# Kernel tuning notes

Measured on AMD Instinct MI355X. Metric: run time of the kernel, lower is better.

Reference implementation:

```python
import jax, jax.numpy as jnp
import numpy as np

LN_EPS = 1e-4
NEG = -1e10


def setup_inputs() -> dict:
    key = jax.random.key(0)
    ks = jax.random.split(key, 5)
    b, p, d, i, h, m = 2, 2048, 1024, 16, 64, 4096
    sd = 1.0 / np.sqrt(d)
    return {
        "x": jax.random.normal(ks[0], (b, p, d), jnp.float32),
        "W_K": jax.random.normal(ks[1], (i, h, d), jnp.float32) * sd,
        "W_Q": jax.random.normal(ks[2], (i, h, d), jnp.float32) * sd,
        "W_V": jax.random.normal(ks[3], (i, h, d), jnp.float32) * sd,
        "w_ln": jnp.ones((d,), jnp.float32),
        "b_ln": jnp.zeros((d,), jnp.float32),
        "W_in": jax.random.normal(ks[4], (m, d), jnp.float32) * sd,
        "b_in": jnp.zeros((m,), jnp.float32),
        "W_out": jax.random.normal(jax.random.fold_in(key, 9), (d, m), jnp.float32) * sd,
        "b_out": jnp.zeros((d,), jnp.float32),
    }


def reference(x, W_K, W_Q, W_V, w_ln, b_ln, W_in, b_in, W_out, b_out):
    b, p, d = x.shape
    # --- attention (unscaled softmax, scaled=False in TransformerBlock) ---
    k = jnp.einsum('ihd,bpd->biph', W_K, x)
    q = jnp.einsum('ihd,bpd->biph', W_Q, x)
    v = jnp.einsum('ihd,bpd->biph', W_V, x)
    scores = jnp.einsum('biph,biqh->biqp', k, q)  # [b,i,q_pos,k_pos]
    causal = jnp.tril(jnp.ones((p, p), bool))      # k_pos <= q_pos
    masked = jnp.where(causal, scores, NEG)
    attn = jax.nn.softmax(masked, axis=-1)
    z = jnp.einsum('biph,biqp->biqh', v, attn)     # [b,i,q,h]
    z_flat = jnp.transpose(z, (0, 2, 1, 3)).reshape(b, p, d)  # b q (i h)
    x = x + z_flat
    # --- custom LayerNorm: unbiased std, eps added to std ---
    c = x - jnp.mean(x, axis=-1, keepdims=True)
    std = jnp.sqrt(jnp.sum(c * c, axis=-1, keepdims=True) / (d - 1))
    x = c / (std + LN_EPS) * w_ln + b_ln
    # --- MLP with residual ---
    hpre = jnp.einsum('md,bpd->bpm', W_in, x) + b_in
    hact = jax.nn.gelu(hpre, approximate=False)
    mlp = jnp.einsum('dm,bpm->bpd', W_out, hact) + b_out
    return x + mlp
```

## Files before the change

kernel.cpp:

```cpp
#include <hip/hip_runtime.h>
#include <hip/hip_bf16.h>

typedef __bf16 bf16x8 __attribute__((ext_vector_type(8)));
typedef float f32x4 __attribute__((ext_vector_type(4)));

#define BAR() __builtin_amdgcn_s_barrier()
#define MEMFENCE() asm volatile("" ::: "memory")
#define VMCNT8() asm volatile("s_waitcnt vmcnt(8)" ::: "memory")
#define VMCNT6() asm volatile("s_waitcnt vmcnt(6)" ::: "memory")
#define VMCNT2() asm volatile("s_waitcnt vmcnt(2)" ::: "memory")
#define VMCNT0() asm volatile("s_waitcnt vmcnt(0)" ::: "memory")

__device__ __forceinline__ void gload_lds16(const void* g, void* l) {
  __builtin_amdgcn_global_load_lds(
      (const __attribute__((address_space(1))) void*)g,
      (__attribute__((address_space(3))) void*)l, 16, 0, 0);
}

__global__ __launch_bounds__(256) void k_f2b_all(
    const float* __restrict__ x, const float* __restrict__ wk,
    const float* __restrict__ wq, const float* __restrict__ wv,
    const float* __restrict__ wi, const float* __restrict__ wo,
    __bf16* __restrict__ xb, __bf16* __restrict__ wqkv,
    __bf16* __restrict__ winb, __bf16* __restrict__ woutb) {
  int i = (blockIdx.x * 256 + threadIdx.x) * 4;
  const float* s; __bf16* d; int off;
  if (i < 4194304)       { s = x;  d = xb;             off = i; }
  else if (i < 5242880)  { s = wk; d = wqkv;           off = i - 4194304; }
  else if (i < 6291456)  { s = wq; d = wqkv + 1048576; off = i - 5242880; }
  else if (i < 7340032)  { s = wv; d = wqkv + 2097152; off = i - 6291456; }
  else if (i < 11534336) { s = wi; d = winb;           off = i - 7340032; }
  else                   { s = wo; d = woutb;          off = i - 11534336; }
  const float4 v = *(const float4*)(s + off);
  d[off + 0] = (__bf16)v.x;
  d[off + 1] = (__bf16)v.y;
  d[off + 2] = (__bf16)v.z;
  d[off + 3] = (__bf16)v.w;
}

template <int EPI, int WM, int WN, int MI, int NI, int SMT, int SNT>
__global__ __launch_bounds__(WM * WN * 64, 2) void k_gemm(
    const __bf16* __restrict__ A, const __bf16* __restrict__ B, int N, int K,
    int NT, const float* __restrict__ bias, const float* __restrict__ resid,
    float* __restrict__ outf, __bf16* __restrict__ outb,
    __bf16* __restrict__ ok, __bf16* __restrict__ oq, __bf16* __restrict__ ovt) {
  constexpr int BM = WM * MI * 16, BN = WN * NI * 16;
  constexpr int LA = BM / (8 * WM * WN);
  constexpr int LB = BN / (8 * WM * WN);
  __shared__ __align__(16) __bf16 lds[2][(BM + BN) * 64];
  const int tid = threadIdx.x;
  const int lane = tid & 63, wid = tid >> 6;
  const int wr = wid / WN, wc = wid % WN;
  const int lr = lane & 15, lh = lane >> 4;
  const int bid = blockIdx.x;
  const int cpx = gridDim.x >> 3;
  const int sid = (bid & 7) * cpx + (bid >> 3);
  const int stn = NT / SNT;
  const int stile = sid / (SMT * SNT);
  const int within = sid - stile * (SMT * SNT);
  const int mt = (stile / stn) * SMT + within / SNT;
  const int nt = (stile % stn) * SNT + within % SNT;
  const int m0 = mt * BM, n0 = nt * BN;
  const int nkt = K >> 6;

  auto stage = [&](int t, int bufi) {
    const int k0 = t << 6;
    __bf16* As = lds[bufi];
    __bf16* Bs = lds[bufi] + BM * 64;
#pragma unroll
    for (int j = 0; j < LA; ++j) {
      int chunk = (wid * LA + j) * 64 + lane;
      int row = chunk >> 3, c8 = chunk & 7;
      int g8 = c8 ^ (row & 7);
      gload_lds16(A + (size_t)(m0 + row) * K + k0 + g8 * 8, As + chunk * 8);
    }
#pragma unroll
    for (int j = 0; j < LB; ++j) {
      int chunk = (wid * LB + j) * 64 + lane;
      int row = chunk >> 3, c8 = chunk & 7;
      int g8 = c8 ^ (row & 7);
      gload_lds16(B + (size_t)(n0 + row) * K + k0 + g8 * 8, Bs + chunk * 8);
    }
  };

  f32x4 acc[MI][NI] = {};
  stage(0, 0);
  stage(1, 1);
  if constexpr (LA + LB == 8) { VMCNT8(); } else { VMCNT6(); }
  BAR();

  for (int t = 0; t < nkt; ++t) {
    const __bf16* As = lds[t & 1];
    const __bf16* Bs = lds[t & 1] + BM * 64;
#pragma unroll
    for (int ks = 0; ks < 2; ++ks) {
      bf16x8 af[MI], bf[NI];
#pragma unroll
      for (int mi = 0; mi < MI; ++mi) {
        int row = wr * (MI * 16) + mi * 16 + lr;
        af[mi] = *(const bf16x8*)&As[row * 64 + (((ks * 4 + lh) ^ (row & 7)) * 8)];
      }
#pragma unroll
      for (int ni = 0; ni < NI; ++ni) {
        int row = wc * (NI * 16) + ni * 16 + lr;
        bf[ni] = *(const bf16x8*)&Bs[row * 64 + (((ks * 4 + lh) ^ (row & 7)) * 8)];
      }
#pragma unroll
      for (int mi = 0; mi < MI; ++mi)
#pragma unroll
        for (int ni = 0; ni < NI; ++ni)
          acc[mi][ni] = __builtin_amdgcn_mfma_f32_16x16x32_bf16(
              af[mi], bf[ni], acc[mi][ni], 0, 0, 0);
    }
    MEMFENCE();
    BAR();
    if (t + 2 < nkt) {
      stage(t + 2, t & 1);
      if constexpr (LA + LB == 8) { VMCNT8(); } else { VMCNT6(); }
    } else {
      VMCNT0();
    }
    BAR();
  }

#pragma unroll
  for (int mi = 0; mi < MI; ++mi) {
#pragma unroll
    for (int j = 0; j < 4; ++j) {
      const int row = m0 + wr * (MI * 16) + mi * 16 + lh * 4 + j;
#pragma unroll
      for (int ni = 0; ni < NI; ++ni) {
        const int col = n0 + wc * (NI * 16) + ni * 16 + lr;
        float v = acc[mi][ni][j];
        if constexpr (EPI == 0) {
          const int which = col >> 10, c = col & 1023;
          const int ih = c >> 6, hh = c & 63;
          const int bb = row >> 11, pp = row & 2047;
          const int bi = bb * 16 + ih;
          if (which == 0)
            ok[((size_t)bi * 2048 + pp) * 64 + hh] = (__bf16)v;
          else if (which == 1)
            oq[((size_t)bi * 2048 + pp) * 64 + hh] = (__bf16)v;
          else
            ovt[((size_t)bi * 64 + hh) * 2048 + pp] = (__bf16)v;
        } else if constexpr (EPI == 1) {
          float h = v + bias[col];
          float g = 0.5f * h * (1.f + erff(h * 0.70710678118f));
          outb[(size_t)row * N + col] = (__bf16)g;
        } else {
          outf[(size_t)row * N + col] = v + bias[col] + resid[(size_t)row * N + col];
        }
      }
    }
  }
}

__global__ __launch_bounds__(512) void k_attn(const __bf16* __restrict__ kb,
                                              const __bf16* __restrict__ qb,
                                              const __bf16* __restrict__ vt,
                                              float* __restrict__ z) {
  const int tid = threadIdx.x;
  const int lane = tid & 63, w = tid >> 6;
  const int lr = lane & 15, lh = lane >> 4;
  const int wgid = blockIdx.x;
  const int xcd = wgid & 7;
  const int t = wgid >> 3;
  const int bi = xcd + 8 * (t & 3);
  const int qblk = t >> 2;
  const int b = bi >> 4, ih = bi & 15;
  const int q0B = qblk * 256;
  const int qw = q0B + w * 32;
  const __bf16* kbase = kb + (size_t)bi * 2048 * 64;
  const __bf16* qbase = qb + (size_t)bi * 2048 * 64;
  const __bf16* vbase = vt + (size_t)bi * 64 * 2048;

  __shared__ __align__(16) __bf16 kv[2][2][64 * 64];
  __shared__ __align__(16) __bf16 plds[8][2][16 * 76];

  const int nk = (q0B >> 6) + 4;

  auto stage = [&](int kt, int bufi) {
    const int k0 = kt << 6;
    const int row = tid >> 3, c8 = tid & 7;
    const int g8 = c8 ^ (row & 7);
    gload_lds16(kbase + (size_t)(k0 + row) * 64 + g8 * 8,
                &kv[bufi][0][tid * 8]);
    gload_lds16(vbase + (size_t)row * 2048 + k0 + g8 * 8,
                &kv[bufi][1][tid * 8]);
  };

  bf16x8 aq[2][2];
#pragma unroll
  for (int tl = 0; tl < 2; ++tl)
#pragma unroll
    for (int ks = 0; ks < 2; ++ks)
      aq[tl][ks] = *(const bf16x8*)(qbase + (size_t)(qw + tl * 16 + lr) * 64 + ks * 32 + lh * 8);

  f32x4 o[2][4] = {};
  float lsum[2][4] = {};

  stage(0, 0);
  stage(1, 1);
  VMCNT2();
  BAR();

  for (int kt = 0; kt < nk; ++kt) {
    const int k0 = kt << 6;
    const __bf16* Ks = kv[kt & 1][0];
    const __bf16* Vs = kv[kt & 1][1];
    const bool act = (k0 <= qw + 31);

    if (act) {
      bf16x8 bk[4][2];
#pragma unroll
      for (int n = 0; n < 4; ++n) {
        int r = n * 16 + lr;
#pragma unroll
        for (int ks = 0; ks < 2; ++ks)
          bk[n][ks] = *(const bf16x8*)&Ks[r * 64 + (((ks * 4 + lh) ^ (r & 7)) * 8)];
      }
      f32x4 s[2][4] = {};
#pragma unroll
      for (int ks = 0; ks < 2; ++ks)
#pragma unroll
        for (int n = 0; n < 4; ++n) {
          s[0][n] = __builtin_amdgcn_mfma_f32_16x16x32_bf16(aq[0][ks], bk[n][ks], s[0][n], 0, 0, 0);
          s[1][n] = __builtin_amdgcn_mfma_f32_16x16x32_bf16(aq[1][ks], bk[n][ks], s[1][n], 0, 0, 0);
        }

      bf16x8 bv[4][2];
#pragma unroll
      for (int ht = 0; ht < 4; ++ht) {
        int r = ht * 16 + lr;
#pragma unroll
        for (int ks = 0; ks < 2; ++ks)
          bv[ht][ks] = *(const bf16x8*)&Vs[r * 64 + (((ks * 4 + lh) ^ (r & 7)) * 8)];
      }

      if (k0 + 63 > qw) {
#pragma unroll
        for (int tl = 0; tl < 2; ++tl)
#pragma unroll
          for (int n = 0; n < 4; ++n)
#pragma unroll
            for (int j = 0; j < 4; ++j) {
              int qpos = qw + tl * 16 + lh * 4 + j;
              int kpos = k0 + n * 16 + lr;
              if (kpos > qpos) s[tl][n][j] = -1e10f;
            }
      }

#pragma unroll
      for (int tl = 0; tl < 2; ++tl) {
#pragma unroll
        for (int n = 0; n < 4; ++n)
#pragma unroll
          for (int j = 0; j < 4; ++j) s[tl][n][j] = __expf(s[tl][n][j]);
#pragma unroll
        for (int j = 0; j < 4; ++j)
          lsum[tl][j] += (s[tl][0][j] + s[tl][1][j]) + (s[tl][2][j] + s[tl][3][j]);
      }

#pragma unroll
      for (int tl = 0; tl < 2; ++tl)
#pragma unroll
        for (int n = 0; n < 4; ++n)
#pragma unroll
          for (int j = 0; j < 4; ++j)
            plds[w][tl][(lh * 4 + j) * 76 + n * 16 + lr] = (__bf16)s[tl][n][j];
      bf16x8 pa[2][2];
#pragma unroll
      for (int tl = 0; tl < 2; ++tl)
#pragma unroll
        for (int ks = 0; ks < 2; ++ks)
          pa[tl][ks] = *(const bf16x8*)&plds[w][tl][lr * 76 + ks * 32 + lh * 8];
#pragma unroll
      for (int ks = 0; ks < 2; ++ks)
#pragma unroll
        for (int ht = 0; ht < 4; ++ht) {
          o[0][ht] = __builtin_amdgcn_mfma_f32_16x16x32_bf16(pa[0][ks], bv[ht][ks], o[0][ht], 0, 0, 0);
          o[1][ht] = __builtin_amdgcn_mfma_f32_16x16x32_bf16(pa[1][ks], bv[ht][ks], o[1][ht], 0, 0, 0);
        }
    }

    MEMFENCE();
    BAR();
    if (kt + 2 < nk) {
      stage(kt + 2, kt & 1);
      VMCNT2();
    } else {
      VMCNT0();
    }
    BAR();
  }

#pragma unroll
  for (int m = 1; m < 16; m <<= 1)
#pragma unroll
    for (int tl = 0; tl < 2; ++tl)
#pragma unroll
      for (int j = 0; j < 4; ++j) lsum[tl][j] += __shfl_xor(lsum[tl][j], m);

  float* zr = z + (size_t)b * 2048 * 1024;
#pragma unroll
  for (int tl = 0; tl < 2; ++tl)
#pragma unroll
    for (int j = 0; j < 4; ++j) {
      float inv = 1.f / lsum[tl][j];
      int q = qw + tl * 16 + lh * 4 + j;
#pragma unroll
      for (int ht = 0; ht < 4; ++ht)
        zr[(size_t)q * 1024 + ih * 64 + ht * 16 + lr] = o[tl][ht][j] * inv;
    }
}

__global__ __launch_bounds__(256) void k_ln(const float* __restrict__ x,
                                            const float* __restrict__ z,
                                            const float* __restrict__ wln,
                                            const float* __restrict__ bln,
                                            float* __restrict__ y,
                                            __bf16* __restrict__ yb) {
  const int row = blockIdx.x;
  const int t = threadIdx.x;
  const int lane = t & 63, wid = t >> 6;
  const float4 xv = ((const float4*)(x + (size_t)row * 1024))[t];
  const float4 zv = ((const float4*)(z + (size_t)row * 1024))[t];
  float v0 = xv.x + zv.x, v1 = xv.y + zv.y, v2 = xv.z + zv.z, v3 = xv.w + zv.w;
  __shared__ float red[4];
  float s = v0 + v1 + v2 + v3;
#pragma unroll
  for (int m = 1; m < 64; m <<= 1) s += __shfl_xor(s, m);
  if (lane == 0) red[wid] = s;
  __syncthreads();
  const float mean = (red[0] + red[1] + red[2] + red[3]) * (1.f / 1024.f);
  const float c0 = v0 - mean, c1 = v1 - mean, c2 = v2 - mean, c3 = v3 - mean;
  float ss = c0 * c0 + c1 * c1 + c2 * c2 + c3 * c3;
#pragma unroll
  for (int m = 1; m < 64; m <<= 1) ss += __shfl_xor(ss, m);
  __syncthreads();
  if (lane == 0) red[wid] = ss;
  __syncthreads();
  const float var = (red[0] + red[1] + red[2] + red[3]) * (1.f / 1023.f);
  const float inv = 1.f / (sqrtf(var) + 1e-4f);
  const float4 wv = ((const float4*)wln)[t];
  const float4 bv = ((const float4*)bln)[t];
  float y0 = c0 * inv * wv.x + bv.x;
  float y1 = c1 * inv * wv.y + bv.y;
  float y2 = c2 * inv * wv.z + bv.z;
  float y3 = c3 * inv * wv.w + bv.w;
  float4 yo; yo.x = y0; yo.y = y1; yo.z = y2; yo.w = y3;
  ((float4*)(y + (size_t)row * 1024))[t] = yo;
  __bf16* yd = yb + (size_t)row * 1024 + t * 4;
  yd[0] = (__bf16)y0; yd[1] = (__bf16)y1; yd[2] = (__bf16)y2; yd[3] = (__bf16)y3;
}

extern "C" void kernel_launch(void* const* d_in, const int* in_sizes, int n_in,
                              void* d_out, int out_size, void* d_ws, size_t ws_size,
                              hipStream_t stream) {
  const float* x = (const float*)d_in[0];
  const float* W_K = (const float*)d_in[1];
  const float* W_Q = (const float*)d_in[2];
  const float* W_V = (const float*)d_in[3];
  const float* w_ln = (const float*)d_in[4];
  const float* b_ln = (const float*)d_in[5];
  const float* W_in = (const float*)d_in[6];
  const float* b_in = (const float*)d_in[7];
  const float* W_out = (const float*)d_in[8];
  const float* b_out = (const float*)d_in[9];
  float* out = (float*)d_out;

  char* ws = (char*)d_ws;
  const size_t NEEDED = 132120576;
  if (ws_size < NEEDED) return;

  __bf16* xb   = (__bf16*)(ws);
  __bf16* wqkv = (__bf16*)(ws + 8388608);
  __bf16* winb = (__bf16*)(ws + 14680064);
  __bf16* woutb= (__bf16*)(ws + 23068672);
  __bf16* kbuf = (__bf16*)(ws + 31457280);
  __bf16* qbuf = (__bf16*)(ws + 39845888);
  __bf16* vtb  = (__bf16*)(ws + 48234496);
  float*  zb   = (float*)(ws + 56623104);
  float*  yf   = (float*)(ws + 73400320);
  __bf16* ybb  = (__bf16*)(ws + 90177536);
  __bf16* hact = (__bf16*)(ws + 98566144);

  k_f2b_all<<<15360, 256, 0, stream>>>(x, W_K, W_Q, W_V, W_in, W_out,
                                       xb, wqkv, winb, woutb);

  k_gemm<0, 2, 2, 4, 4, 4, 4><<<768, 256, 0, stream>>>(
      xb, wqkv, 3072, 1024, 24, nullptr, nullptr, nullptr, nullptr,
      kbuf, qbuf, vtb);
  k_attn<<<dim3(256), 512, 0, stream>>>(kbuf, qbuf, vtb, zb);
  k_ln<<<4096, 256, 0, stream>>>(x, zb, w_ln, b_ln, yf, ybb);
  k_gemm<1, 2, 2, 4, 4, 4, 4><<<1024, 256, 0, stream>>>(
      ybb, winb, 4096, 1024, 32, b_in, nullptr, nullptr, hact,
      nullptr, nullptr, nullptr);
  k_gemm<2, 2, 2, 4, 2, 2, 2><<<512, 256, 0, stream>>>(
      hact, woutb, 1024, 4096, 16, b_out, yf, out, nullptr,
      nullptr, nullptr, nullptr);
}
```

Baseline: 214.0 us.

## Halve attention query tile per block and launch heaviest causal blocks first

The attention kernel now gives each wave 16 query rows instead of 32, so a block covers 128 queries and the grid doubles to 512 workgroups. Block indices are mapped in reverse so the blocks with the longest causal key ranges are scheduled first, which should even out the tail. The intent is more parallelism and better load balance across CUs. The cost is that each K/V tile staged in LDS is reused by fewer query rows, so global and LDS traffic per unit of work rises.

```diff
diff --git a/kernel.cpp b/kernel.cpp
--- a/kernel.cpp
+++ b/kernel.cpp
@@ -165,19 +165,18 @@
   const int wgid = blockIdx.x;
   const int xcd = wgid & 7;
   const int t = wgid >> 3;
+  const int c = 15 - (t >> 2);
   const int bi = xcd + 8 * (t & 3);
-  const int qblk = t >> 2;
   const int b = bi >> 4, ih = bi & 15;
-  const int q0B = qblk * 256;
-  const int qw = q0B + w * 32;
+  const int qw = c * 128 + w * 16;
   const __bf16* kbase = kb + (size_t)bi * 2048 * 64;
   const __bf16* qbase = qb + (size_t)bi * 2048 * 64;
   const __bf16* vbase = vt + (size_t)bi * 64 * 2048;
 
   __shared__ __align__(16) __bf16 kv[2][2][64 * 64];
-  __shared__ __align__(16) __bf16 plds[8][2][16 * 76];
-
-  const int nk = (q0B >> 6) + 4;
+  __shared__ __align__(16) __bf16 plds[8][16 * 76];
+
+  const int nk = 2 * c + 2;
 
   auto stage = [&](int kt, int bufi) {
     const int k0 = kt << 6;
@@ -189,15 +188,13 @@
                 &kv[bufi][1][tid * 8]);
   };
 
-  bf16x8 aq[2][2];
-#pragma unroll
-  for (int tl = 0; tl < 2; ++tl)
-#pragma unroll
-    for (int ks = 0; ks < 2; ++ks)
-      aq[tl][ks] = *(const bf16x8*)(qbase + (size_t)(qw + tl * 16 + lr) * 64 + ks * 32 + lh * 8);
-
-  f32x4 o[2][4] = {};
-  float lsum[2][4] = {};
+  bf16x8 aq[2];
+#pragma unroll
+  for (int ks = 0; ks < 2; ++ks)
+    aq[ks] = *(const bf16x8*)(qbase + (size_t)(qw + lr) * 64 + ks * 32 + lh * 8);
+
+  f32x4 o[4] = {};
+  float lsum[4] = {0.f, 0.f, 0.f, 0.f};
 
   stage(0, 0);
   stage(1, 1);
@@ -208,7 +205,7 @@
     const int k0 = kt << 6;
     const __bf16* Ks = kv[kt & 1][0];
     const __bf16* Vs = kv[kt & 1][1];
-    const bool act = (k0 <= qw + 31);
+    const bool act = (k0 <= qw + 15);
 
     if (act) {
       bf16x8 bk[4][2];
@@ -219,14 +216,12 @@
         for (int ks = 0; ks < 2; ++ks)
           bk[n][ks] = *(const bf16x8*)&Ks[r * 64 + (((ks * 4 + lh) ^ (r & 7)) * 8)];
       }
-      f32x4 s[2][4] = {};
+      f32x4 s[4] = {};
 #pragma unroll
       for (int ks = 0; ks < 2; ++ks)
 #pragma unroll
-        for (int n = 0; n < 4; ++n) {
-          s[0][n] = __builtin_amdgcn_mfma_f32_16x16x32_bf16(aq[0][ks], bk[n][ks], s[0][n], 0, 0, 0);
-          s[1][n] = __builtin_amdgcn_mfma_f32_16x16x32_bf16(aq[1][ks], bk[n][ks], s[1][n], 0, 0, 0);
-        }
+        for (int n = 0; n < 4; ++n)
+          s[n] = __builtin_amdgcn_mfma_f32_16x16x32_bf16(aq[ks], bk[n][ks], s[n], 0, 0, 0);
 
       bf16x8 bv[4][2];
 #pragma unroll
@@ -239,48 +234,37 @@
 
       if (k0 + 63 > qw) {
 #pragma unroll
-        for (int tl = 0; tl < 2; ++tl)
-#pragma unroll
-          for (int n = 0; n < 4; ++n)
-#pragma unroll
-            for (int j = 0; j < 4; ++j) {
-              int qpos = qw + tl * 16 + lh * 4 + j;
-              int kpos = k0 + n * 16 + lr;
-              if (kpos > qpos) s[tl][n][j] = -1e10f;
-            }
-      }
-
-#pragma unroll
-      for (int tl = 0; tl < 2; ++tl) {
-#pragma unroll
         for (int n = 0; n < 4; ++n)
 #pragma unroll
-          for (int j = 0; j < 4; ++j) s[tl][n][j] = __expf(s[tl][n][j]);
+          for (int j = 0; j < 4; ++j) {
+            int qpos = qw + lh * 4 + j;
+            int kpos = k0 + n * 16 + lr;
+            if (kpos > qpos) s[n][j] = -1e10f;
+          }
+      }
+
+#pragma unroll
+      for (int n = 0; n < 4; ++n)
+#pragma unroll
+        for (int j = 0; j < 4; ++j) s[n][j] = __expf(s[n][j]);
+#pragma unroll
+      for (int j = 0; j < 4; ++j)
+        lsum[j] += (s[0][j] + s[1][j]) + (s[2][j] + s[3][j]);
+
+#pragma unroll
+      for (int n = 0; n < 4; ++n)
 #pragma unroll
         for (int j = 0; j < 4; ++j)
-          lsum[tl][j] += (s[tl][0][j] + s[tl][1][j]) + (s[tl][2][j] + s[tl][3][j]);
-      }
-
-#pragma unroll
-      for (int tl = 0; tl < 2; ++tl)
-#pragma unroll
-        for (int n = 0; n < 4; ++n)
-#pragma unroll
-          for (int j = 0; j < 4; ++j)
-            plds[w][tl][(lh * 4 + j) * 76 + n * 16 + lr] = (__bf16)s[tl][n][j];
-      bf16x8 pa[2][2];
-#pragma unroll
-      for (int tl = 0; tl < 2; ++tl)
-#pragma unroll
-        for (int ks = 0; ks < 2; ++ks)
-          pa[tl][ks] = *(const bf16x8*)&plds[w][tl][lr * 76 + ks * 32 + lh * 8];
+          plds[w][(lh * 4 + j) * 76 + n * 16 + lr] = (__bf16)s[n][j];
+      bf16x8 pa[2];
 #pragma unroll
       for (int ks = 0; ks < 2; ++ks)
-#pragma unroll
-        for (int ht = 0; ht < 4; ++ht) {
-          o[0][ht] = __builtin_amdgcn_mfma_f32_16x16x32_bf16(pa[0][ks], bv[ht][ks], o[0][ht], 0, 0, 0);
-          o[1][ht] = __builtin_amdgcn_mfma_f32_16x16x32_bf16(pa[1][ks], bv[ht][ks], o[1][ht], 0, 0, 0);
-        }
+        pa[ks] = *(const bf16x8*)&plds[w][lr * 76 + ks * 32 + lh * 8];
+#pragma unroll
+      for (int ks = 0; ks < 2; ++ks)
+#pragma unroll
+        for (int ht = 0; ht < 4; ++ht)
+          o[ht] = __builtin_amdgcn_mfma_f32_16x16x32_bf16(pa[ks], bv[ht][ks], o[ht], 0, 0, 0);
     }
 
     MEMFENCE();
@@ -297,21 +281,17 @@
 #pragma unroll
   for (int m = 1; m < 16; m <<= 1)
 #pragma unroll
-    for (int tl = 0; tl < 2; ++tl)
-#pragma unroll
-      for (int j = 0; j < 4; ++j) lsum[tl][j] += __shfl_xor(lsum[tl][j], m);
+    for (int j = 0; j < 4; ++j) lsum[j] += __shfl_xor(lsum[j], m);
 
   float* zr = z + (size_t)b * 2048 * 1024;
 #pragma unroll
-  for (int tl = 0; tl < 2; ++tl)
-#pragma unroll
-    for (int j = 0; j < 4; ++j) {
-      float inv = 1.f / lsum[tl][j];
-      int q = qw + tl * 16 + lh * 4 + j;
-#pragma unroll
-      for (int ht = 0; ht < 4; ++ht)
-        zr[(size_t)q * 1024 + ih * 64 + ht * 16 + lr] = o[tl][ht][j] * inv;
-    }
+  for (int j = 0; j < 4; ++j) {
+    float inv = 1.f / lsum[j];
+    int q = qw + lh * 4 + j;
+#pragma unroll
+    for (int ht = 0; ht < 4; ++ht)
+      zr[(size_t)q * 1024 + ih * 64 + ht * 16 + lr] = o[ht][j] * inv;
+  }
 }
 
 __global__ __launch_bounds__(256) void k_ln(const float* __restrict__ x,
@@ -391,7 +371,7 @@
   k_gemm<0, 2, 2, 4, 4, 4, 4><<<768, 256, 0, stream>>>(
       xb, wqkv, 3072, 1024, 24, nullptr, nullptr, nullptr, nullptr,
       kbuf, qbuf, vtb);
-  k_attn<<<dim3(256), 512, 0, stream>>>(kbuf, qbuf, vtb, zb);
+  k_attn<<<dim3(512), 512, 0, stream>>>(kbuf, qbuf, vtb, zb);
   k_ln<<<4096, 256, 0, stream>>>(x, zb, w_ln, b_ln, yf, ybb);
   k_gemm<1, 2, 2, 4, 4, 4, 4><<<1024, 256, 0, stream>>>(
       ybb, winb, 4096, 1024, 32, b_in, nullptr, nullptr, hact,
```

New measurement: 198.6 us. 1.08x faster.
